# Optimization experiments

Hardware: AMD Instinct MI355X
Metric: run time of the kernel (lower is better)

## Reference

```python
import jax, jax.numpy as jnp
import numpy as np

N_HEAD = 8
LN_EPS = 1e-5


def _layer_norm(x, g, b):
    mu = jnp.mean(x, axis=-1, keepdims=True)
    var = jnp.mean(jnp.square(x - mu), axis=-1, keepdims=True)
    return (x - mu) * jax.lax.rsqrt(var + LN_EPS) * g + b


def _pos_encoding(L, d, dtype):
    pos = jnp.arange(L, dtype=jnp.float32)[:, None]                      # [L,1]
    div = jnp.exp(jnp.arange(0, d, 2, dtype=jnp.float32) * (-np.log(10000.0) / d))  # [d/2]
    # interleave sin (even idx) / cos (odd idx)
    pe = jnp.stack([jnp.sin(pos * div), jnp.cos(pos * div)], axis=-1).reshape(L, d)
    return pe.astype(dtype)


def setup_inputs() -> dict:
    key = jax.random.key(0)
    B, L, D, F, NL = 256, 100, 512, 2048, 4
    ks = jax.random.split(key, 8)
    s = lambda fan_in: 1.0 / np.sqrt(fan_in)
    return {
        "x": jax.random.normal(ks[0], (B, L, D), dtype=jnp.float32),
        "mask": jnp.ones((B, L), dtype=jnp.int32),
        # weights stored as [in, out] (torch Linear weight transposed)
        "qkv_w": jax.random.uniform(ks[1], (NL, D, 3 * D), minval=-s(D), maxval=s(D)),
        "fc_w": jax.random.uniform(ks[2], (NL, D, D), minval=-s(D), maxval=s(D)),
        "fc_b": jnp.zeros((NL, D), dtype=jnp.float32),
        "ln1_g": jnp.ones((NL, D), dtype=jnp.float32),
        "ln1_b": jnp.zeros((NL, D), dtype=jnp.float32),
        "ln2_g": jnp.ones((NL, D), dtype=jnp.float32),
        "ln2_b": jnp.zeros((NL, D), dtype=jnp.float32),
        "ffn_w1": jax.random.uniform(ks[3], (NL, D, F), minval=-s(D), maxval=s(D)),
        "ffn_b1": jnp.zeros((NL, F), dtype=jnp.float32),
        "ffn_w2": jax.random.uniform(ks[4], (NL, F, D), minval=-s(F), maxval=s(F)),
        "ffn_b2": jnp.zeros((NL, D), dtype=jnp.float32),
    }


def _attn(x, mask, qkv_w, fc_w, fc_b):
    B, L, D = x.shape
    hd = D // N_HEAD
    qkv = x @ qkv_w                                      # [B,L,3D]
    q, k, v = jnp.split(qkv, 3, axis=-1)
    q = q.reshape(B, L, N_HEAD, hd).transpose(0, 2, 1, 3)   # [B,H,L,hd]
    k = k.reshape(B, L, N_HEAD, hd).transpose(0, 2, 1, 3)
    v = v.reshape(B, L, N_HEAD, hd).transpose(0, 2, 1, 3)
    scores = jnp.einsum("bhqd,bhkd->bhqk", q, k)          # scale=1 (scale=False)
    scores = jnp.where(mask[:, None, None, :] == 0, -jnp.inf, scores)
    attn = jax.nn.softmax(scores, axis=-1)
    out = jnp.einsum("bhqk,bhkd->bhqd", attn, v)
    out = out.transpose(0, 2, 1, 3).reshape(B, L, D)
    return out @ fc_w + fc_b


def reference(x, mask, qkv_w, fc_w, fc_b, ln1_g, ln1_b, ln2_g, ln2_b,
              ffn_w1, ffn_b1, ffn_w2, ffn_b2):
    B, L, D = x.shape
    pe = _pos_encoding(L, D, x.dtype)                     # [L,D]
    # pos_embed: x = x + (x + pe)  (dropout is identity at eval)
    x = x + (x + pe[None, :, :])
    n_layers = qkv_w.shape[0]
    for i in range(n_layers):  # post-norm (after_norm=True)
        res = x
        x = _attn(x, mask, qkv_w[i], fc_w[i], fc_b[i])
        x = _layer_norm(x + res, ln1_g[i], ln1_b[i])
        res = x
        h = jax.nn.relu(x @ ffn_w1[i] + ffn_b1[i])
        x = _layer_norm(res + (h @ ffn_w2[i] + ffn_b2[i]), ln2_g[i], ln2_b[i])
    return x
```

## Files before the change

### kernel.cpp

```cpp
#include <hip/hip_runtime.h>
#include <cstdint>
#include <cmath>


#define NLAYERS 4
#define BB 256
#define LL 100
#define DD 512
#define FF 2048
#define NH 8
#define HD 64
#define MM (BB*LL)
#define ATT_R 112
#define ATT_K 128

typedef __bf16 bf16;
typedef bf16 bf16x8 __attribute__((ext_vector_type(8)));
typedef bf16 bf16x4 __attribute__((ext_vector_type(4)));
typedef float f32x4 __attribute__((ext_vector_type(4)));

__device__ __forceinline__ void load16(const void* g, void* l) {
  __builtin_amdgcn_global_load_lds(
      (const __attribute__((address_space(1))) void*)g,
      (__attribute__((address_space(3))) void*)l, 16, 0, 0);
}

__global__ void pe_kernel(float* __restrict__ pe) {
  const int idx = blockIdx.x * 256 + threadIdx.x;
  if (idx >= LL * DD) return;
  const int l = idx >> 9, d = idx & 511;
  const int i = d >> 1;
  const float div = expf((float)(2 * i) * (-9.210340371976184f / 512.f));
  const float ang = (float)l * div;
  pe[idx] = (d & 1) ? cosf(ang) : sinf(ang);
}

__global__ __launch_bounds__(256) void x0_kernel(
    const float* __restrict__ xin, const float* __restrict__ pe,
    bf16* __restrict__ XB) {
  const size_t f = (size_t)blockIdx.x * 256 + threadIdx.x;
  const size_t e = f << 2;
  const int col  = (int)(e & 511);
  const int prow = (int)((e >> 9) % LL);
  const float4 xv = *(const float4*)(xin + e);
  const float4 pv = *(const float4*)(pe + (size_t)prow * DD + col);
  bf16x4 pk;
  pk[0] = (bf16)(2.f * xv.x + pv.x);
  pk[1] = (bf16)(2.f * xv.y + pv.y);
  pk[2] = (bf16)(2.f * xv.z + pv.z);
  pk[3] = (bf16)(2.f * xv.w + pv.w);
  *(bf16x4*)(XB + e) = pk;
}

__global__ void transpose_cast(const float* __restrict__ src, bf16* __restrict__ dst,
                               int K, int N) {
  __shared__ float tile[32][33];
  const int z = blockIdx.z;
  src += (size_t)z * K * N;
  dst += (size_t)z * K * N;
  const int k0 = blockIdx.y * 32, n0 = blockIdx.x * 32;
  const int tx = threadIdx.x, ty = threadIdx.y;
  #pragma unroll
  for (int i = 0; i < 32; i += 8)
    tile[ty + i][tx] = src[(size_t)(k0 + ty + i) * N + n0 + tx];
  __syncthreads();
  #pragma unroll
  for (int i = 0; i < 32; i += 8)
    dst[(size_t)(n0 + ty + i) * K + k0 + tx] = (bf16)tile[tx][ty + i];
}

__device__ __forceinline__ bf16x8 lds_frag(const bf16* chunk, int lrow, int cb) {
  return *(const bf16x8*)(chunk + (lrow << 6) + ((cb ^ (lrow & 7)) << 3));
}

__device__ __forceinline__ void stage4(const bf16* g, size_t r32, bf16* chunk, int w) {
  load16(g,            chunk + (w << 9));
  load16(g + r32,      chunk + 2048 + (w << 9));
  load16(g + 2 * r32,  chunk + 4096 + (w << 9));
  load16(g + 3 * r32,  chunk + 6144 + (w << 9));
}

template<int OUT_BF16, int RELU>
__global__ __launch_bounds__(256, 2) void gemm128(
    const bf16* __restrict__ A, const bf16* __restrict__ Bt,
    const float* __restrict__ bias, void* __restrict__ Cv,
    int N, int K) {
  __shared__ __align__(16) bf16 sA[2][128 * 64];
  __shared__ __align__(16) bf16 sB[2][128 * 64];
  const int tid = threadIdx.x;
  const int w = tid >> 6, lane = tid & 63;
  const int wr = w >> 1, wc = w & 1;
  const int lr16 = lane & 15, lg = lane >> 4;
  const int NT = K >> 6;

  const int nwg = gridDim.x * gridDim.y;
  const int orig = blockIdx.y * gridDim.x + blockIdx.x;
  const int q = nwg >> 3, r = nwg & 7;
  const int xcd = orig & 7, lo = orig >> 3;
  const int swz = (xcd < r ? xcd * (q + 1) : r * (q + 1) + (xcd - r) * q) + lo;
  const int bn = (swz % gridDim.x) << 7;
  const int bm = (swz / gridDim.x) << 7;

  const int rr0 = tid >> 3;
  const int cb  = (tid & 7) ^ (rr0 & 7);
  const bf16* gA = A  + (size_t)(bm + rr0) * K + (cb << 3);
  const bf16* gB = Bt + (size_t)(bn + rr0) * K + (cb << 3);
  const size_t r32 = (size_t)32 * K;

  f32x4 acc[4][4] = {};
  bf16x8 Af[4][2], Bf[4][2];

  stage4(gA,      r32, sA[0], w);
  stage4(gB,      r32, sB[0], w);
  stage4(gA + 64, r32, sA[1], w);
  stage4(gB + 64, r32, sB[1], w);

  for (int t = 0; t < NT; ++t) {
    const int cur = t & 1;
    if (t < NT - 1) asm volatile("s_waitcnt vmcnt(8)" ::: "memory");
    else            asm volatile("s_waitcnt vmcnt(0)" ::: "memory");
    __builtin_amdgcn_s_barrier();

    #pragma unroll
    for (int m = 0; m < 4; ++m) {
      const int lrow = wr * 64 + m * 16 + lr16;
      Af[m][0] = lds_frag(sA[cur], lrow, lg);
      Af[m][1] = lds_frag(sA[cur], lrow, 4 + lg);
    }
    #pragma unroll
    for (int n = 0; n < 4; ++n) {
      const int lrow = wc * 64 + n * 16 + lr16;
      Bf[n][0] = lds_frag(sB[cur], lrow, lg);
      Bf[n][1] = lds_frag(sB[cur], lrow, 4 + lg);
    }
    __builtin_amdgcn_s_barrier();

    if (t + 2 < NT) stage4(gA + (size_t)(t + 2) * 64, r32, sA[cur], w);
    __builtin_amdgcn_s_setprio(1);
    #pragma unroll
    for (int m = 0; m < 4; ++m)
      #pragma unroll
      for (int n = 0; n < 4; ++n)
        acc[m][n] = __builtin_amdgcn_mfma_f32_16x16x32_bf16(Af[m][0], Bf[n][0], acc[m][n], 0, 0, 0);
    __builtin_amdgcn_s_setprio(0);
    if (t + 2 < NT) stage4(gB + (size_t)(t + 2) * 64, r32, sB[cur], w);
    __builtin_amdgcn_s_setprio(1);
    #pragma unroll
    for (int m = 0; m < 4; ++m)
      #pragma unroll
      for (int n = 0; n < 4; ++n)
        acc[m][n] = __builtin_amdgcn_mfma_f32_16x16x32_bf16(Af[m][1], Bf[n][1], acc[m][n], 0, 0, 0);
    __builtin_amdgcn_s_setprio(0);
  }

  const int g4 = (lane >> 4) << 2;
  #pragma unroll
  for (int n = 0; n < 4; ++n) {
    const int col = bn + wc * 64 + n * 16 + lr16;
    const float bvv = bias ? bias[col] : 0.f;
    #pragma unroll
    for (int m = 0; m < 4; ++m) {
      const int row = bm + wr * 64 + m * 16 + g4;
      #pragma unroll
      for (int j = 0; j < 4; ++j) {
        float v = acc[m][n][j] + bvv;
        if (RELU) v = fmaxf(v, 0.f);
        if (OUT_BF16) ((bf16*)Cv)[(size_t)(row + j) * N + col] = (bf16)v;
        else          ((float*)Cv)[(size_t)(row + j) * N + col] = v;
      }
    }
  }
}

__global__ __launch_bounds__(256) void attn_mfma(
    const bf16* __restrict__ qkv, const int* __restrict__ mask,
    bf16* __restrict__ aout) {
  __shared__ __align__(16) bf16 sQ[ATT_R * 64];
  __shared__ __align__(16) bf16 sK[ATT_R * 64];
  __shared__ __align__(16) bf16 sVt[64 * 136];
  __shared__ __align__(16) bf16 sP[ATT_R * ATT_K];
  __shared__ int sM[ATT_R];
  const int bh = blockIdx.x, b = bh >> 3, h = bh & 7;
  const int tid = threadIdx.x, w = tid >> 6, lane = tid & 63;
  const int lr = lane & 15;
  const int lk = (lane >> 4) << 3;
  const int g  = lane >> 4;

  for (int i = tid; i < ATT_R * 64 / 8; i += 256) { ((int4*)sQ)[i] = int4{0,0,0,0}; ((int4*)sK)[i] = int4{0,0,0,0}; }
  for (int i = tid; i < 64 * 136 / 8; i += 256) ((int4*)sVt)[i] = int4{0,0,0,0};
  for (int i = tid; i < ATT_R * ATT_K / 8; i += 256) ((int4*)sP)[i] = int4{0,0,0,0};
  __syncthreads();

  const bf16* base = qkv + (size_t)(b * LL) * (3 * DD) + h * HD;
  for (int c = tid; c < LL * 8; c += 256) {
    const int l = c >> 3, u = c & 7;
    const bf16x8 qv = *(const bf16x8*)(base + (size_t)l * (3 * DD) + u * 8);
    const bf16x8 kv = *(const bf16x8*)(base + (size_t)l * (3 * DD) + DD + u * 8);
    const bf16x8 vv = *(const bf16x8*)(base + (size_t)l * (3 * DD) + 2 * DD + u * 8);
    const int qb = (l * 128 + u * 16) ^ ((l & 7) << 4);
    *(bf16x8*)((char*)sQ + qb) = qv;
    *(bf16x8*)((char*)sK + qb) = kv;
    #pragma unroll
    for (int j = 0; j < 8; ++j) sVt[(u * 8 + j) * 136 + l] = vv[j];
  }
  if (tid < ATT_R) sM[tid] = (tid < LL) ? mask[b * LL + tid] : 0;
  __syncthreads();

  #pragma unroll
  for (int fi = 0; fi < 2; ++fi) {
    const int fm = w + fi * 4;
    if (fm >= 7) continue;
    const int ar = fm * 16 + lr;
    const int abase = ar * 128;
    const int aswz = (ar & 7) << 4;
    const bf16x8 a0 = *(const bf16x8*)((char*)sQ + ((abase + lk * 2) ^ aswz));
    const bf16x8 a1 = *(const bf16x8*)((char*)sQ + ((abase + 64 + lk * 2) ^ aswz));
    f32x4 s[7];
    #pragma unroll
    for (int fn = 0; fn < 7; ++fn) {
      const int br = fn * 16 + lr;
      const int bswz = (br & 7) << 4;
      const bf16x8 b0 = *(const bf16x8*)((char*)sK + ((br * 128 + lk * 2) ^ bswz));
      const bf16x8 b1 = *(const bf16x8*)((char*)sK + ((br * 128 + 64 + lk * 2) ^ bswz));
      f32x4 acc = {};
      acc = __builtin_amdgcn_mfma_f32_16x16x32_bf16(a0, b0, acc, 0, 0, 0);
      acc = __builtin_amdgcn_mfma_f32_16x16x32_bf16(a1, b1, acc, 0, 0, 0);
      s[fn] = acc;
    }
    #pragma unroll
    for (int fn = 0; fn < 7; ++fn) {
      if (sM[fn * 16 + lr] == 0) {
        s[fn][0] = -INFINITY; s[fn][1] = -INFINITY;
        s[fn][2] = -INFINITY; s[fn][3] = -INFINITY;
      }
    }
    float sm[4];
    #pragma unroll
    for (int j = 0; j < 4; ++j) {
      float m = s[0][j];
      #pragma unroll
      for (int fn = 1; fn < 7; ++fn) m = fmaxf(m, s[fn][j]);
      #pragma unroll
      for (int off = 1; off < 16; off <<= 1) m = fmaxf(m, __shfl_xor(m, off, 64));
      float t = 0.f;
      #pragma unroll
      for (int fn = 0; fn < 7; ++fn) { const float p = __expf(s[fn][j] - m); s[fn][j] = p; t += p; }
      #pragma unroll
      for (int off = 1; off < 16; off <<= 1) t += __shfl_xor(t, off, 64);
      sm[j] = 1.f / t;
    }
    #pragma unroll
    for (int fn = 0; fn < 7; ++fn) {
      const int k = fn * 16 + lr;
      #pragma unroll
      for (int j = 0; j < 4; ++j) {
        const int rr = fm * 16 + 4 * g + j;
        const int byte = (rr * 256 + k * 2) ^ ((rr & 7) << 4);
        *(bf16*)((char*)sP + byte) = (bf16)(s[fn][j] * sm[j]);
      }
    }
  }
  __syncthreads();

  bf16x8 bV[4];
  #pragma unroll
  for (int ks = 0; ks < 4; ++ks)
    bV[ks] = *(const bf16x8*)((char*)sVt + ((w * 16 + lr) * 272 + ks * 64 + lk * 2));
  #pragma unroll
  for (int fm = 0; fm < 7; ++fm) {
    f32x4 acc = {};
    const int ar = fm * 16 + lr;
    const int aswz = (ar & 7) << 4;
    #pragma unroll
    for (int ks = 0; ks < 4; ++ks) {
      const bf16x8 aP = *(const bf16x8*)((char*)sP + ((ar * 256 + ks * 64 + lk * 2) ^ aswz));
      acc = __builtin_amdgcn_mfma_f32_16x16x32_bf16(aP, bV[ks], acc, 0, 0, 0);
    }
    const int d = h * HD + w * 16 + lr;
    #pragma unroll
    for (int j = 0; j < 4; ++j) {
      const int qr = fm * 16 + 4 * g + j;
      if (qr < LL) aout[(size_t)(b * LL + qr) * DD + d] = (bf16)acc[j];
    }
  }
}

template<int WRITE_F32>
__global__ __launch_bounds__(256) void ln_kernel(
    const float* __restrict__ Y, const bf16* __restrict__ RES,
    const float* __restrict__ g, const float* __restrict__ bt,
    bf16* __restrict__ XB, float* __restrict__ XF) {
  const int row = blockIdx.x * 4 + (threadIdx.x >> 6);
  const int lane = threadIdx.x & 63;
  const size_t base = (size_t)row * DD + lane * 8;
  const float4 a0 = *(const float4*)(Y + base);
  const float4 a1 = *(const float4*)(Y + base + 4);
  const bf16x8 rv = *(const bf16x8*)(RES + base);
  float z[8];
  z[0] = a0.x + (float)rv[0]; z[1] = a0.y + (float)rv[1];
  z[2] = a0.z + (float)rv[2]; z[3] = a0.w + (float)rv[3];
  z[4] = a1.x + (float)rv[4]; z[5] = a1.y + (float)rv[5];
  z[6] = a1.z + (float)rv[6]; z[7] = a1.w + (float)rv[7];
  float s = 0.f, s2 = 0.f;
  #pragma unroll
  for (int j = 0; j < 8; ++j) { s += z[j]; s2 = fmaf(z[j], z[j], s2); }
  #pragma unroll
  for (int off = 32; off > 0; off >>= 1) {
    s  += __shfl_xor(s, off, 64);
    s2 += __shfl_xor(s2, off, 64);
  }
  const float mu = s * (1.f / 512.f);
  const float var = s2 * (1.f / 512.f) - mu * mu;
  const float inv = rsqrtf(var + 1e-5f);
  const int c = lane * 8;
  const float4 g0 = *(const float4*)(g + c),  g1 = *(const float4*)(g + c + 4);
  const float4 b0 = *(const float4*)(bt + c), b1 = *(const float4*)(bt + c + 4);
  float ov[8];
  ov[0] = (z[0] - mu) * inv * g0.x + b0.x; ov[1] = (z[1] - mu) * inv * g0.y + b0.y;
  ov[2] = (z[2] - mu) * inv * g0.z + b0.z; ov[3] = (z[3] - mu) * inv * g0.w + b0.w;
  ov[4] = (z[4] - mu) * inv * g1.x + b1.x; ov[5] = (z[5] - mu) * inv * g1.y + b1.y;
  ov[6] = (z[6] - mu) * inv * g1.z + b1.z; ov[7] = (z[7] - mu) * inv * g1.w + b1.w;
  bf16x8 pk;
  #pragma unroll
  for (int j = 0; j < 8; ++j) pk[j] = (bf16)ov[j];
  *(bf16x8*)(XB + base) = pk;
  if (WRITE_F32) {
    *(float4*)(XF + base)     = make_float4(ov[0], ov[1], ov[2], ov[3]);
    *(float4*)(XF + base + 4) = make_float4(ov[4], ov[5], ov[6], ov[7]);
  }
}

extern "C" void kernel_launch(void* const* d_in, const int* in_sizes, int n_in,
                              void* d_out, int out_size, void* d_ws, size_t ws_size,
                              hipStream_t stream) {
  const float* x_in   = (const float*)d_in[0];
  const int*   mask   = (const int*)d_in[1];
  const float* qkv_w  = (const float*)d_in[2];
  const float* fc_w   = (const float*)d_in[3];
  const float* fc_b   = (const float*)d_in[4];
  const float* ln1_g  = (const float*)d_in[5];
  const float* ln1_b  = (const float*)d_in[6];
  const float* ln2_g  = (const float*)d_in[7];
  const float* ln2_b  = (const float*)d_in[8];
  const float* ffn_w1 = (const float*)d_in[9];
  const float* ffn_b1 = (const float*)d_in[10];
  const float* ffn_w2 = (const float*)d_in[11];
  const float* ffn_b2 = (const float*)d_in[12];

  char* ws = (char*)d_ws;
  size_t off = 0;
  auto alloc = [&](size_t bytes) -> void* {
    off = (off + 255) & ~(size_t)255;
    void* p = ws + off;
    off += bytes;
    return p;
  };
  bf16*  XB   = (bf16*) alloc((size_t)MM * DD * 2);
  bf16*  BIGB = (bf16*) alloc((size_t)MM * FF * 2);
  float* PE   = (float*)alloc((size_t)LL * DD * 4);
  bf16*  WQKV = (bf16*) alloc((size_t)NLAYERS * DD * 3 * DD * 2);
  bf16*  WFC  = (bf16*) alloc((size_t)NLAYERS * DD * DD * 2);
  bf16*  W1T  = (bf16*) alloc((size_t)NLAYERS * DD * FF * 2);
  bf16*  W2T  = (bf16*) alloc((size_t)NLAYERS * FF * DD * 2);
  bf16*  AOUT = BIGB + (size_t)MM * (3 * DD);
  float* Y    = (float*)d_out;
  (void)ws_size; (void)in_sizes; (void)n_in; (void)out_size;

  pe_kernel<<<200, 256, 0, stream>>>(PE);
  transpose_cast<<<dim3(48, 16, NLAYERS), dim3(32, 8), 0, stream>>>(qkv_w,  WQKV, 512, 1536);
  transpose_cast<<<dim3(16, 16, NLAYERS), dim3(32, 8), 0, stream>>>(fc_w,   WFC,  512, 512);
  transpose_cast<<<dim3(64, 16, NLAYERS), dim3(32, 8), 0, stream>>>(ffn_w1, W1T,  512, 2048);
  transpose_cast<<<dim3(16, 64, NLAYERS), dim3(32, 8), 0, stream>>>(ffn_w2, W2T,  2048, 512);
  x0_kernel<<<12800, 256, 0, stream>>>(x_in, PE, XB);

  for (int i = 0; i < NLAYERS; ++i) {
    gemm128<1, 0><<<dim3(12, 200), 256, 0, stream>>>(
        XB, WQKV + (size_t)i * DD * 3 * DD, nullptr, BIGB, 3 * DD, DD);
    attn_mfma<<<BB * NH, 256, 0, stream>>>(BIGB, mask, AOUT);
    gemm128<0, 0><<<dim3(4, 200), 256, 0, stream>>>(
        AOUT, WFC + (size_t)i * DD * DD, fc_b + i * DD, Y, DD, DD);
    ln_kernel<0><<<MM / 4, 256, 0, stream>>>(Y, XB, ln1_g + i * DD, ln1_b + i * DD, XB, nullptr);
    gemm128<1, 1><<<dim3(16, 200), 256, 0, stream>>>(
        XB, W1T + (size_t)i * DD * FF, ffn_b1 + i * FF, BIGB, FF, DD);
    gemm128<0, 0><<<dim3(4, 200), 256, 0, stream>>>(
        BIGB, W2T + (size_t)i * FF * DD, ffn_b2 + i * DD, Y, DD, FF);
    if (i == NLAYERS - 1)
      ln_kernel<1><<<MM / 4, 256, 0, stream>>>(Y, XB, ln2_g + i * DD, ln2_b + i * DD,
                                               XB, (float*)d_out);
    else
      ln_kernel<0><<<MM / 4, 256, 0, stream>>>(Y, XB, ln2_g + i * DD, ln2_b + i * DD, XB, nullptr);
  }
}
```

Before: 1.126 ms.

## Switch GEMM to 32x32x16 MFMA and fuse residual add into epilogue

```diff
diff --git a/kernel.cpp b/kernel.cpp
--- a/kernel.cpp
+++ b/kernel.cpp
@@ -18,6 +18,7 @@
 typedef bf16 bf16x8 __attribute__((ext_vector_type(8)));
 typedef bf16 bf16x4 __attribute__((ext_vector_type(4)));
 typedef float f32x4 __attribute__((ext_vector_type(4)));
+typedef float f32x16 __attribute__((ext_vector_type(16)));
 
 __device__ __forceinline__ void load16(const void* g, void* l) {
   __builtin_amdgcn_global_load_lds(
@@ -80,17 +81,17 @@
   load16(g + 3 * r32,  chunk + 6144 + (w << 9));
 }
 
-template<int OUT_BF16, int RELU>
+template<int OUT_BF16, int RELU, int RESID>
 __global__ __launch_bounds__(256, 2) void gemm128(
     const bf16* __restrict__ A, const bf16* __restrict__ Bt,
-    const float* __restrict__ bias, void* __restrict__ Cv,
-    int N, int K) {
+    const float* __restrict__ bias, const bf16* __restrict__ RES,
+    void* __restrict__ Cv, int N, int K) {
   __shared__ __align__(16) bf16 sA[2][128 * 64];
   __shared__ __align__(16) bf16 sB[2][128 * 64];
   const int tid = threadIdx.x;
   const int w = tid >> 6, lane = tid & 63;
   const int wr = w >> 1, wc = w & 1;
-  const int lr16 = lane & 15, lg = lane >> 4;
+  const int l31 = lane & 31, l5 = lane >> 5;
   const int NT = K >> 6;
 
   const int nwg = gridDim.x * gridDim.y;
@@ -107,8 +108,8 @@
   const bf16* gB = Bt + (size_t)(bn + rr0) * K + (cb << 3);
   const size_t r32 = (size_t)32 * K;
 
-  f32x4 acc[4][4] = {};
-  bf16x8 Af[4][2], Bf[4][2];
+  f32x16 acc[2][2] = {};
+  bf16x8 Af[2][4], Bf[2][4];
 
   stage4(gA,      r32, sA[0], w);
   stage4(gB,      r32, sB[0], w);
@@ -122,51 +123,54 @@
     __builtin_amdgcn_s_barrier();
 
     #pragma unroll
-    for (int m = 0; m < 4; ++m) {
-      const int lrow = wr * 64 + m * 16 + lr16;
-      Af[m][0] = lds_frag(sA[cur], lrow, lg);
-      Af[m][1] = lds_frag(sA[cur], lrow, 4 + lg);
-    }
-    #pragma unroll
-    for (int n = 0; n < 4; ++n) {
-      const int lrow = wc * 64 + n * 16 + lr16;
-      Bf[n][0] = lds_frag(sB[cur], lrow, lg);
-      Bf[n][1] = lds_frag(sB[cur], lrow, 4 + lg);
-    }
+    for (int m = 0; m < 2; ++m)
+      #pragma unroll
+      for (int ks = 0; ks < 4; ++ks)
+        Af[m][ks] = lds_frag(sA[cur], wr * 64 + m * 32 + l31, ks * 2 + l5);
+    #pragma unroll
+    for (int n = 0; n < 2; ++n)
+      #pragma unroll
+      for (int ks = 0; ks < 4; ++ks)
+        Bf[n][ks] = lds_frag(sB[cur], wc * 64 + n * 32 + l31, ks * 2 + l5);
     __builtin_amdgcn_s_barrier();
 
     if (t + 2 < NT) stage4(gA + (size_t)(t + 2) * 64, r32, sA[cur], w);
     __builtin_amdgcn_s_setprio(1);
     #pragma unroll
-    for (int m = 0; m < 4; ++m)
-      #pragma unroll
-      for (int n = 0; n < 4; ++n)
-        acc[m][n] = __builtin_amdgcn_mfma_f32_16x16x32_bf16(Af[m][0], Bf[n][0], acc[m][n], 0, 0, 0);
+    for (int m = 0; m < 2; ++m)
+      #pragma unroll
+      for (int n = 0; n < 2; ++n) {
+        acc[m][n] = __builtin_amdgcn_mfma_f32_32x32x16_bf16(Af[m][0], Bf[n][0], acc[m][n], 0, 0, 0);
+        acc[m][n] = __builtin_amdgcn_mfma_f32_32x32x16_bf16(Af[m][1], Bf[n][1], acc[m][n], 0, 0, 0);
+      }
     __builtin_amdgcn_s_setprio(0);
     if (t + 2 < NT) stage4(gB + (size_t)(t + 2) * 64, r32, sB[cur], w);
     __builtin_amdgcn_s_setprio(1);
     #pragma unroll
-    for (int m = 0; m < 4; ++m)
-      #pragma unroll
-      for (int n = 0; n < 4; ++n)
-        acc[m][n] = __builtin_amdgcn_mfma_f32_16x16x32_bf16(Af[m][1], Bf[n][1], acc[m][n], 0, 0, 0);
+    for (int m = 0; m < 2; ++m)
+      #pragma unroll
+      for (int n = 0; n < 2; ++n) {
+        acc[m][n] = __builtin_amdgcn_mfma_f32_32x32x16_bf16(Af[m][2], Bf[n][2], acc[m][n], 0, 0, 0);
+        acc[m][n] = __builtin_amdgcn_mfma_f32_32x32x16_bf16(Af[m][3], Bf[n][3], acc[m][n], 0, 0, 0);
+      }
     __builtin_amdgcn_s_setprio(0);
   }
 
-  const int g4 = (lane >> 4) << 2;
-  #pragma unroll
-  for (int n = 0; n < 4; ++n) {
-    const int col = bn + wc * 64 + n * 16 + lr16;
+  #pragma unroll
+  for (int n = 0; n < 2; ++n) {
+    const int col = bn + wc * 64 + n * 32 + l31;
     const float bvv = bias ? bias[col] : 0.f;
     #pragma unroll
-    for (int m = 0; m < 4; ++m) {
-      const int row = bm + wr * 64 + m * 16 + g4;
-      #pragma unroll
-      for (int j = 0; j < 4; ++j) {
-        float v = acc[m][n][j] + bvv;
+    for (int m = 0; m < 2; ++m) {
+      const int rbase = bm + wr * 64 + m * 32 + 4 * l5;
+      #pragma unroll
+      for (int rr = 0; rr < 16; ++rr) {
+        const int row = rbase + (rr & 3) + 8 * (rr >> 2);
+        float v = acc[m][n][rr] + bvv;
         if (RELU) v = fmaxf(v, 0.f);
-        if (OUT_BF16) ((bf16*)Cv)[(size_t)(row + j) * N + col] = (bf16)v;
-        else          ((float*)Cv)[(size_t)(row + j) * N + col] = v;
+        if (RESID) v += (float)RES[(size_t)row * N + col];
+        if (OUT_BF16) ((bf16*)Cv)[(size_t)row * N + col] = (bf16)v;
+        else          ((float*)Cv)[(size_t)row * N + col] = v;
       }
     }
   }
@@ -287,7 +291,7 @@
 
 template<int WRITE_F32>
 __global__ __launch_bounds__(256) void ln_kernel(
-    const float* __restrict__ Y, const bf16* __restrict__ RES,
+    const float* __restrict__ Y,
     const float* __restrict__ g, const float* __restrict__ bt,
     bf16* __restrict__ XB, float* __restrict__ XF) {
   const int row = blockIdx.x * 4 + (threadIdx.x >> 6);
@@ -295,12 +299,7 @@
   const size_t base = (size_t)row * DD + lane * 8;
   const float4 a0 = *(const float4*)(Y + base);
   const float4 a1 = *(const float4*)(Y + base + 4);
-  const bf16x8 rv = *(const bf16x8*)(RES + base);
-  float z[8];
-  z[0] = a0.x + (float)rv[0]; z[1] = a0.y + (float)rv[1];
-  z[2] = a0.z + (float)rv[2]; z[3] = a0.w + (float)rv[3];
-  z[4] = a1.x + (float)rv[4]; z[5] = a1.y + (float)rv[5];
-  z[6] = a1.z + (float)rv[6]; z[7] = a1.w + (float)rv[7];
+  float z[8] = {a0.x, a0.y, a0.z, a0.w, a1.x, a1.y, a1.z, a1.w};
   float s = 0.f, s2 = 0.f;
   #pragma unroll
   for (int j = 0; j < 8; ++j) { s += z[j]; s2 = fmaf(z[j], z[j], s2); }
@@ -374,20 +373,20 @@
   x0_kernel<<<12800, 256, 0, stream>>>(x_in, PE, XB);
 
   for (int i = 0; i < NLAYERS; ++i) {
-    gemm128<1, 0><<<dim3(12, 200), 256, 0, stream>>>(
-        XB, WQKV + (size_t)i * DD * 3 * DD, nullptr, BIGB, 3 * DD, DD);
+    gemm128<1, 0, 0><<<dim3(12, 200), 256, 0, stream>>>(
+        XB, WQKV + (size_t)i * DD * 3 * DD, nullptr, nullptr, BIGB, 3 * DD, DD);
     attn_mfma<<<BB * NH, 256, 0, stream>>>(BIGB, mask, AOUT);
-    gemm128<0, 0><<<dim3(4, 200), 256, 0, stream>>>(
-        AOUT, WFC + (size_t)i * DD * DD, fc_b + i * DD, Y, DD, DD);
-    ln_kernel<0><<<MM / 4, 256, 0, stream>>>(Y, XB, ln1_g + i * DD, ln1_b + i * DD, XB, nullptr);
-    gemm128<1, 1><<<dim3(16, 200), 256, 0, stream>>>(
-        XB, W1T + (size_t)i * DD * FF, ffn_b1 + i * FF, BIGB, FF, DD);
-    gemm128<0, 0><<<dim3(4, 200), 256, 0, stream>>>(
-        BIGB, W2T + (size_t)i * FF * DD, ffn_b2 + i * DD, Y, DD, FF);
+    gemm128<0, 0, 1><<<dim3(4, 200), 256, 0, stream>>>(
+        AOUT, WFC + (size_t)i * DD * DD, fc_b + i * DD, XB, Y, DD, DD);
+    ln_kernel<0><<<MM / 4, 256, 0, stream>>>(Y, ln1_g + i * DD, ln1_b + i * DD, XB, nullptr);
+    gemm128<1, 1, 0><<<dim3(16, 200), 256, 0, stream>>>(
+        XB, W1T + (size_t)i * DD * FF, ffn_b1 + i * FF, nullptr, BIGB, FF, DD);
+    gemm128<0, 0, 1><<<dim3(4, 200), 256, 0, stream>>>(
+        BIGB, W2T + (size_t)i * FF * DD, ffn_b2 + i * DD, XB, Y, DD, FF);
     if (i == NLAYERS - 1)
-      ln_kernel<1><<<MM / 4, 256, 0, stream>>>(Y, XB, ln2_g + i * DD, ln2_b + i * DD,
+      ln_kernel<1><<<MM / 4, 256, 0, stream>>>(Y, ln2_g + i * DD, ln2_b + i * DD,
                                                XB, (float*)d_out);
     else
-      ln_kernel<0><<<MM / 4, 256, 0, stream>>>(Y, XB, ln2_g + i * DD, ln2_b + i * DD, XB, nullptr);
-  }
-}
+      ln_kernel<0><<<MM / 4, 256, 0, stream>>>(Y, ln2_g + i * DD, ln2_b + i * DD, XB, nullptr);
+  }
+}
```

New measurement: 1.171 ms. 4.0% more time.
